# Performance work log

Hardware: AMD Instinct MI355X
Metric: run time of the kernel (lower is better)

Reference implementation:

```python
import jax, jax.numpy as jnp
from jax import lax
import numpy as np

LEVEL_HW = [(100, 100), (50, 50), (25, 25), (13, 13), (7, 7)]  # P3..P7 for 800x800 input
N, C, A, K, NCONV = 2, 256, 9, 80, 4
PRIOR_PROB = 0.01


def conv3x3(x, w, b):
    # x: (N,C,H,W), w: (O,I,3,3), stride 1, pad 1
    y = lax.conv_general_dilated(x, w, (1, 1), 'SAME',
                                 dimension_numbers=('NCHW', 'OIHW', 'NCHW'))
    return y + b[None, :, None, None]


def permute_to_N_HWA_K(t, k):
    # (N, A*k, H, W) -> (N, H*W*A, k), matching the torch helper
    n, _, h, w = t.shape
    return t.reshape(n, -1, k, h, w).transpose(0, 3, 4, 1, 2).reshape(n, -1, k)


def setup_inputs() -> dict:
    key = jax.random.key(0)
    ks = iter(jax.random.split(key, 64))
    inp = {}
    for i, (h, w) in enumerate(LEVEL_HW):
        inp[f"f{i}"] = jax.random.normal(next(ks), (N, C, h, w), jnp.float32)
    for pre in ("cls", "box"):
        for i in range(NCONV):
            inp[f"{pre}_w{i}"] = 0.01 * jax.random.normal(next(ks), (C, C, 3, 3), jnp.float32)
            inp[f"{pre}_b{i}"] = jnp.zeros((C,), jnp.float32)
    bias_value = -float(np.log((1.0 - PRIOR_PROB) / PRIOR_PROB))
    inp["cls_score_w"] = 0.01 * jax.random.normal(next(ks), (A * K, C, 3, 3), jnp.float32)
    inp["cls_score_b"] = jnp.full((A * K,), bias_value, jnp.float32)
    inp["box_pred_w"] = 0.01 * jax.random.normal(next(ks), (A * 4, C, 3, 3), jnp.float32)
    inp["box_pred_b"] = jnp.zeros((A * 4,), jnp.float32)
    return inp


def reference(f0, f1, f2, f3, f4,
              cls_w0, cls_b0, cls_w1, cls_b1, cls_w2, cls_b2, cls_w3, cls_b3,
              box_w0, box_b0, box_w1, box_b1, box_w2, box_b2, box_w3, box_b3,
              cls_score_w, cls_score_b, box_pred_w, box_pred_b):
    feats = [f0, f1, f2, f3, f4]
    cls_p = [(cls_w0, cls_b0), (cls_w1, cls_b1), (cls_w2, cls_b2), (cls_w3, cls_b3)]
    box_p = [(box_w0, box_b0), (box_w1, box_b1), (box_w2, box_b2), (box_w3, box_b3)]
    logits, boxes = [], []
    for f in feats:
        x = f
        for w, b in cls_p:
            x = jax.nn.relu(conv3x3(x, w, b))
        logits.append(permute_to_N_HWA_K(conv3x3(x, cls_score_w, cls_score_b), K))
        y = f
        for w, b in box_p:
            y = jax.nn.relu(conv3x3(y, w, b))
        boxes.append(permute_to_N_HWA_K(conv3x3(y, box_pred_w, box_pred_b), 4))
    # (N, R, K) and (N, R, 4) with R = sum_l Hl*Wl*A = 120087; concat on last dim
    return jnp.concatenate([jnp.concatenate(logits, 1), jnp.concatenate(boxes, 1)], axis=2)
```

## Files before the change

### kernel.cpp

```cpp
#include <hip/hip_runtime.h>


typedef __attribute__((ext_vector_type(8))) short short8;
typedef __attribute__((ext_vector_type(4))) float floatx4;

#define LVLTOT 14143

__device__ __forceinline__ unsigned short f2bf(float f) {
  unsigned int u = __float_as_uint(f);
  unsigned int r = (u + 0x7fffu + ((u >> 16) & 1u)) >> 16;
  return (unsigned short)r;
}

__device__ __forceinline__ void gload_lds16(const void* g, void* l) {
  __builtin_amdgcn_global_load_lds(
      (const __attribute__((address_space(1))) unsigned int*)g,
      (__attribute__((address_space(3))) unsigned int*)l, 16, 0, 0);
}

struct PrepArgs {
  const float* f[5];
  const float* w[10];
  unsigned short* wdst[10];
  int wblk_off[11];
  int cout[10];
  unsigned short* x0;
  unsigned short* bufA;
  unsigned short* bufB;
};

__global__ __launch_bounds__(256) void prep(PrepArgs A) {
  static const int Ht[5] = {100, 50, 25, 13, 7};
  static const int Wpt[5] = {102, 52, 27, 15, 9};
  static const int LOFFt[5] = {0, 10404, 13108, 13837, 14062};
  __shared__ float ts[32][33];
  const int bid = blockIdx.x;
  const int t = threadIdx.x;

  if (bid < 1090) {
    int sid = bid % 545, n = bid / 545;
    int l, h, wb;
    if (sid < 400)      { l = 0; h = sid >> 2; wb = sid & 3; }
    else if (sid < 500) { l = 1; h = (sid - 400) >> 1; wb = (sid - 400) & 1; }
    else if (sid < 525) { l = 2; h = sid - 500; wb = 0; }
    else if (sid < 538) { l = 3; h = sid - 525; wb = 0; }
    else                { l = 4; h = sid - 538; wb = 0; }
    const float* f = A.f[l];
    int H = Ht[l], W = H, Wp = Wpt[l], loff = LOFFt[l];
    int w0 = wb * 32;
    for (int s = 0; s < 8; s++) {
      int ch0 = s * 32;
      __syncthreads();
#pragma unroll
      for (int r4 = 0; r4 < 4; r4++) {
        int ch = ch0 + (t >> 5) + r4 * 8;
        int px = w0 + (t & 31);
        float v = 0.f;
        if (px < W) v = f[(((size_t)n * 256 + ch) * H + h) * W + px];
        ts[(t >> 5) + r4 * 8][t & 31] = v;
      }
      __syncthreads();
      int pxl = t >> 3, c4 = t & 7;
      if (w0 + pxl < W) {
        unsigned short pk[4];
#pragma unroll
        for (int k = 0; k < 4; k++) pk[k] = f2bf(ts[c4 * 4 + k][pxl]);
        *(unsigned long long*)(A.x0 +
            ((size_t)n * LVLTOT + loff + (size_t)(h + 1) * Wp + (w0 + pxl + 1)) *
                256 + ch0 + c4 * 4) = *(unsigned long long*)pk;
      }
    }
    return;
  }

  if (bid < 3970) {
    int b2 = bid - 1090;
    int tix = 0;
    while (b2 >= A.wblk_off[tix + 1]) tix++;
    int co = b2 - A.wblk_off[tix];
    int ci = t;
    bool valid = co < A.cout[tix];
    const float* w = A.w[tix];
    unsigned short* dst = A.wdst[tix];
    int cb = co >> 6, col = co & 63, chk = ci >> 5, qd = (ci >> 3) & 3, j = ci & 7;
#pragma unroll
    for (int tap = 0; tap < 9; tap++) {
      float v = valid ? w[((size_t)co * 256 + ci) * 9 + tap] : 0.f;
      dst[((((size_t)(cb * 8 + chk) * 9 + tap) * 4 + qd) * 64 + col) * 8 + j] =
          f2bf(v);
    }
    return;
  }

  {
    static const int BCUM[6] = {0, 404, 608, 712, 768, 800};
    int b3 = bid - 3970;
    int plane = b3 / 100;
    int item = (b3 % 100) * 256 + t;
    int pxi = item >> 5, oct = item & 31;
    if (pxi >= 800) return;
    int l = 0;
    while (pxi >= BCUM[l + 1]) l++;
    int j = pxi - BCUM[l];
    int Wp = Wpt[l];
    int r, c;
    if (j < Wp)            { r = 0; c = j; }
    else if (j < 2 * Wp)   { r = Wp - 1; c = j - Wp; }
    else { int k = j - 2 * Wp; r = 1 + (k >> 1); c = (k & 1) ? Wp - 1 : 0; }
    size_t px = (size_t)LOFFt[l] + (size_t)r * Wp + c;
    unsigned short* base = (plane < 4)
                               ? (A.bufA + (size_t)plane * LVLTOT * 256)
                               : (A.bufB + (size_t)(plane - 4) * LVLTOT * 256);
    floatx4 z;
    z[0] = z[1] = z[2] = z[3] = 0.f;
    *(floatx4*)(base + px * 256 + oct * 8) = z;
  }
}

__device__ __forceinline__ void decode_tile(int tile, int& l, int& h0, int& w0,
                                            int& H, int& W, int& Wp, int& loff) {
  const int Ht[5] = {100, 50, 25, 13, 7};
  const int Wpt[5] = {102, 52, 27, 15, 9};
  const int TXt[5] = {7, 4, 2, 1, 1};
  const int LOFFt[5] = {0, 10404, 13108, 13837, 14062};
  int tloc;
  if (tile < 49) { l = 0; tloc = tile; }
  else if (tile < 65) { l = 1; tloc = tile - 49; }
  else if (tile < 69) { l = 2; tloc = tile - 65; }
  else if (tile < 70) { l = 3; tloc = tile - 69; }
  else { l = 4; tloc = 0; }
  H = Ht[l]; W = H; Wp = Wpt[l]; loff = LOFFt[l];
  int ty = tloc / TXt[l], tx = tloc - ty * TXt[l];
  h0 = ty * 16; w0 = tx * 16;
}

#define CONV_MAIN_LOOP(INP, WBLOB, CB)                                         \
  {                                                                            \
    size_t xoff[6];                                                            \
    _Pragma("unroll") for (int g = 0; g < 6; g++) {                            \
      int px = g * 64 + lane;                                                  \
      int r = px / 18, c = px - r * 18;                                        \
      int hh = h0 + r; if (hh > Hpad - 1) hh = Hpad - 1;                       \
      int ww = w0 + c; if (ww > Wp - 1) ww = Wp - 1;                           \
      xoff[g] = ((size_t)hh * Wp + ww) * 256 + wv * 8;                         \
    }                                                                          \
    for (int ch = 0; ch < 8; ch++) {                                           \
      if (ch) __syncthreads();                                                 \
      const unsigned short* wsrc = (WBLOB) + ((size_t)((CB)*8 + ch)) * 18432;  \
      _Pragma("unroll") for (int i = 0; i < 9; i++)                            \
        gload_lds16(wsrc + i * 2048 + wv * 512 + lane * 8,                     \
                    lds_w + i * 2048 + wv * 512);                              \
      _Pragma("unroll") for (int g = 0; g < 6; g++)                            \
        gload_lds16((INP) + xoff[g] + ch * 32, lds_x + wv * 3072 + g * 512);   \
      __syncthreads();                                                         \
      const short8* xw = (const short8*)lds_w;                                 \
      const short8* xx = (const short8*)lds_x;                                 \
      _Pragma("unroll") for (int tdx = 0; tdx < 3; tdx++) {                    \
        short8 bfr[6];                                                         \
        _Pragma("unroll") for (int rw = 0; rw < 6; rw++)                       \
          bfr[rw] = xx[q * 384 + (wv * 4 + rw) * 18 + n16 + tdx];              \
        _Pragma("unroll") for (int tdy = 0; tdy < 3; tdy++) {                  \
          const int tap = tdy * 3 + tdx;                                       \
          _Pragma("unroll") for (int cc = 0; cc < 4; cc++) {                   \
            short8 afr = xw[(tap * 4 + q) * 64 + cc * 16 + n16];               \
            _Pragma("unroll") for (int rr = 0; rr < 4; rr++)                   \
              acc[cc][rr] = __builtin_amdgcn_mfma_f32_16x16x32_bf16(           \
                  afr, bfr[rr + tdy], acc[cc][rr], 0, 0, 0);                   \
          }                                                                    \
        }                                                                      \
      }                                                                        \
    }                                                                          \
  }

__global__ __launch_bounds__(256, 2) void conv_tower_mfma(
    const unsigned short* __restrict__ xin, unsigned short* __restrict__ xout,
    const unsigned short* __restrict__ wblob_cls,
    const unsigned short* __restrict__ wblob_box,
    const float* __restrict__ bias_cls, const float* __restrict__ bias_box,
    int in_n_stride, int in_tw_stride) {
  __shared__ __align__(16) unsigned short lds_w[18432];
  __shared__ __align__(16) unsigned short lds_x[12288];
  const int t = threadIdx.x, lane = t & 63, wv = t >> 6;
  const int q = lane >> 4, n16 = lane & 15;
  int l, h0, w0, H, W, Wp, loff;
  decode_tile(blockIdx.x, l, h0, w0, H, W, Wp, loff);
  const int Hpad = H + 2;
  const int cb = blockIdx.y;
  const int n = blockIdx.z >> 1, tw = blockIdx.z & 1;
  const unsigned short* wblob = tw ? wblob_box : wblob_cls;
  const float* bias = tw ? bias_box : bias_cls;
  const unsigned short* inp =
      xin + ((size_t)n * in_n_stride + (size_t)tw * in_tw_stride + loff) * 256;
  unsigned short* outp = xout + ((size_t)(n * 2 + tw) * LVLTOT + loff) * 256;

  floatx4 acc[4][4];
#pragma unroll
  for (int i = 0; i < 4; i++)
#pragma unroll
    for (int jj = 0; jj < 4; jj++) acc[i][jj] = (floatx4){0.f, 0.f, 0.f, 0.f};

  CONV_MAIN_LOOP(inp, wblob, cb)

#pragma unroll
  for (int cc = 0; cc < 4; cc++) {
    floatx4 bb = *(const floatx4*)(bias + cb * 64 + cc * 16 + q * 4);
#pragma unroll
    for (int rr = 0; rr < 4; rr++) {
      int h = h0 + wv * 4 + rr;
      int w_ = w0 + n16;
      if (h < H && w_ < W) {
        unsigned short pk[4];
#pragma unroll
        for (int rg = 0; rg < 4; rg++)
          pk[rg] = f2bf(fmaxf(acc[cc][rr][rg] + bb[rg], 0.f));
        size_t base =
            ((size_t)(h + 1) * Wp + (w_ + 1)) * 256 + cb * 64 + cc * 16 + q * 4;
        *(unsigned long long*)(outp + base) = *(unsigned long long*)pk;
      }
    }
  }
}

__global__ __launch_bounds__(256, 2) void conv_final_mfma(
    const unsigned short* __restrict__ xin, float* __restrict__ out,
    const unsigned short* __restrict__ wblob_cls,
    const unsigned short* __restrict__ wblob_box,
    const float* __restrict__ bias_cls, const float* __restrict__ bias_box) {
  __shared__ __align__(16) unsigned short lds_w[18432];
  __shared__ __align__(16) unsigned short lds_x[12288];
  const int t = threadIdx.x, lane = t & 63, wv = t >> 6;
  const int q = lane >> 4, n16 = lane & 15;
  int l, h0, w0, H, W, Wp, loff;
  decode_tile(blockIdx.x, l, h0, w0, H, W, Wp, loff);
  const int Hpad = H + 2;
  const int yb = blockIdx.y;
  const bool is_cls = yb < 12;
  const int cb = is_cls ? yb : 0;
  const int tw = is_cls ? 0 : 1;
  const int Cout = is_cls ? 720 : 36;
  const unsigned short* wblob = is_cls ? wblob_cls : wblob_box;
  const float* bias = is_cls ? bias_cls : bias_box;
  const int n = blockIdx.z;
  const int RB[5] = {0, 90000, 112500, 118125, 119646};
  const unsigned short* inp = xin + ((size_t)(n * 2 + tw) * LVLTOT + loff) * 256;

  floatx4 acc[4][4];
#pragma unroll
  for (int i = 0; i < 4; i++)
#pragma unroll
    for (int jj = 0; jj < 4; jj++) acc[i][jj] = (floatx4){0.f, 0.f, 0.f, 0.f};

  CONV_MAIN_LOOP(inp, wblob, cb)

#pragma unroll
  for (int cc = 0; cc < 4; cc++) {
    int co0 = cb * 64 + cc * 16 + q * 4;
    if (co0 >= Cout) continue;
    floatx4 bb = *(const floatx4*)(bias + co0);
    int a = is_cls ? (co0 / 80) : (co0 >> 2);
    int col0 = is_cls ? (co0 - a * 80) : 80;
#pragma unroll
    for (int rr = 0; rr < 4; rr++) {
      int h = h0 + wv * 4 + rr;
      int w_ = w0 + n16;
      if (h < H && w_ < W) {
        size_t ridx = (size_t)RB[l] + ((size_t)h * W + w_) * 9 + a;
        floatx4 v;
#pragma unroll
        for (int rg = 0; rg < 4; rg++) v[rg] = acc[cc][rr][rg] + bb[rg];
        *(floatx4*)(out + ((size_t)n * 120087 + ridx) * 84 + col0) = v;
      }
    }
  }
}

extern "C" void kernel_launch(void* const* d_in, const int* in_sizes, int n_in,
                              void* d_out, int out_size, void* d_ws,
                              size_t ws_size, hipStream_t stream) {
  char* ws = (char*)d_ws;
  unsigned short* bufB = (unsigned short*)(ws);
  unsigned short* X0 = (unsigned short*)(ws + 14482432);
  unsigned short* bufA = (unsigned short*)(ws + 28964864);
  unsigned short* tb[8];
  for (int i = 0; i < 8; i++)
    tb[i] = (unsigned short*)(ws + 57929728 + (size_t)i * 1179648);
  unsigned short* fb_cls = (unsigned short*)(ws + 67366912);
  unsigned short* fb_box = (unsigned short*)(ws + 70905856);

  float* out = (float*)d_out;

  PrepArgs pa;
  for (int i = 0; i < 5; i++) pa.f[i] = (const float*)d_in[i];
  for (int i = 0; i < 4; i++) {
    pa.w[i] = (const float*)d_in[5 + 2 * i];
    pa.w[4 + i] = (const float*)d_in[13 + 2 * i];
    pa.wdst[i] = tb[i];
    pa.wdst[4 + i] = tb[4 + i];
    pa.cout[i] = pa.cout[4 + i] = 256;
  }
  pa.w[8] = (const float*)d_in[21]; pa.wdst[8] = fb_cls; pa.cout[8] = 720;
  pa.w[9] = (const float*)d_in[23]; pa.wdst[9] = fb_box; pa.cout[9] = 36;
  int off = 0;
  for (int i = 0; i < 8; i++) { pa.wblk_off[i] = off; off += 256; }
  pa.wblk_off[8] = off; off += 768;
  pa.wblk_off[9] = off; off += 64;
  pa.wblk_off[10] = off;
  pa.x0 = X0;
  pa.bufA = bufA;
  pa.bufB = bufB;

  prep<<<dim3(4770), 256, 0, stream>>>(pa);

  const float *cls_b[4], *box_b[4];
  for (int i = 0; i < 4; i++) {
    cls_b[i] = (const float*)d_in[6 + 2 * i];
    box_b[i] = (const float*)d_in[14 + 2 * i];
  }

  dim3 gt(71, 4, 4);
  conv_tower_mfma<<<gt, 256, 0, stream>>>(X0, bufA, tb[0], tb[4], cls_b[0],
                                          box_b[0], LVLTOT, 0);
  conv_tower_mfma<<<gt, 256, 0, stream>>>(bufA, bufB, tb[1], tb[5], cls_b[1],
                                          box_b[1], 2 * LVLTOT, LVLTOT);
  conv_tower_mfma<<<gt, 256, 0, stream>>>(bufB, bufA, tb[2], tb[6], cls_b[2],
                                          box_b[2], 2 * LVLTOT, LVLTOT);
  conv_tower_mfma<<<gt, 256, 0, stream>>>(bufA, bufB, tb[3], tb[7], cls_b[3],
                                          box_b[3], 2 * LVLTOT, LVLTOT);

  conv_final_mfma<<<dim3(71, 13, 2), 256, 0, stream>>>(
      bufB, out, fb_cls, fb_box, (const float*)d_in[22], (const float*)d_in[24]);
}
```

Baseline: 638.5 us.

## Double-buffer LDS staging in conv main loop to overlap loads with MFMA

Splits the conv main loop into separate stage and compute macros and ping-pongs two LDS buffers, so the global-to-LDS loads for the next channel chunk are issued while MFMAs run on the current chunk. This halves the barriers per chunk pair and aims to hide global load latency. LDS use per block doubles to about 120 KB and the launch bounds drop the two-blocks-per-CU hint, so occupancy likely falls to one block per CU.

```diff
diff --git a/kernel.cpp b/kernel.cpp
--- a/kernel.cpp
+++ b/kernel.cpp
@@ -134,6 +134,37 @@
   h0 = ty * 16; w0 = tx * 16;
 }
 
+#define CONV_STAGE(INP, WBLOB, CB, CH, LW, LX)                                 \
+  {                                                                            \
+    const unsigned short* wsrc =                                               \
+        (WBLOB) + ((size_t)((CB) * 8 + (CH))) * 18432;                         \
+    _Pragma("unroll") for (int i = 0; i < 9; i++)                              \
+      gload_lds16(wsrc + i * 2048 + wv * 512 + lane * 8,                       \
+                  (LW) + i * 2048 + wv * 512);                                 \
+    _Pragma("unroll") for (int g = 0; g < 6; g++)                              \
+      gload_lds16((INP) + xoff[g] + (CH) * 32, (LX) + wv * 3072 + g * 512);    \
+  }
+
+#define CONV_COMPUTE(LW, LX)                                                   \
+  {                                                                            \
+    const short8* xw = (const short8*)(LW);                                    \
+    const short8* xx = (const short8*)(LX);                                    \
+    _Pragma("unroll") for (int tdx = 0; tdx < 3; tdx++) {                      \
+      short8 bfr[6];                                                           \
+      _Pragma("unroll") for (int rw = 0; rw < 6; rw++)                         \
+        bfr[rw] = xx[q * 384 + (wv * 4 + rw) * 18 + n16 + tdx];                \
+      _Pragma("unroll") for (int tdy = 0; tdy < 3; tdy++) {                    \
+        const int tap = tdy * 3 + tdx;                                         \
+        _Pragma("unroll") for (int cc = 0; cc < 4; cc++) {                     \
+          short8 afr = xw[(tap * 4 + q) * 64 + cc * 16 + n16];                 \
+          _Pragma("unroll") for (int rr = 0; rr < 4; rr++)                     \
+            acc[cc][rr] = __builtin_amdgcn_mfma_f32_16x16x32_bf16(             \
+                afr, bfr[rr + tdy], acc[cc][rr], 0, 0, 0);                     \
+        }                                                                      \
+      }                                                                        \
+    }                                                                          \
+  }
+
 #define CONV_MAIN_LOOP(INP, WBLOB, CB)                                         \
   {                                                                            \
     size_t xoff[6];                                                            \
@@ -144,42 +175,28 @@
       int ww = w0 + c; if (ww > Wp - 1) ww = Wp - 1;                           \
       xoff[g] = ((size_t)hh * Wp + ww) * 256 + wv * 8;                         \
     }                                                                          \
-    for (int ch = 0; ch < 8; ch++) {                                           \
-      if (ch) __syncthreads();                                                 \
-      const unsigned short* wsrc = (WBLOB) + ((size_t)((CB)*8 + ch)) * 18432;  \
-      _Pragma("unroll") for (int i = 0; i < 9; i++)                            \
-        gload_lds16(wsrc + i * 2048 + wv * 512 + lane * 8,                     \
-                    lds_w + i * 2048 + wv * 512);                              \
-      _Pragma("unroll") for (int g = 0; g < 6; g++)                            \
-        gload_lds16((INP) + xoff[g] + ch * 32, lds_x + wv * 3072 + g * 512);   \
+    CONV_STAGE(INP, WBLOB, CB, 0, lds_w[0], lds_x[0])                          \
+    __syncthreads();                                                           \
+    for (int cp = 0; cp < 4; cp++) {                                           \
+      CONV_STAGE(INP, WBLOB, CB, 2 * cp + 1, lds_w[1], lds_x[1])               \
+      CONV_COMPUTE(lds_w[0], lds_x[0])                                         \
       __syncthreads();                                                         \
-      const short8* xw = (const short8*)lds_w;                                 \
-      const short8* xx = (const short8*)lds_x;                                 \
-      _Pragma("unroll") for (int tdx = 0; tdx < 3; tdx++) {                    \
-        short8 bfr[6];                                                         \
-        _Pragma("unroll") for (int rw = 0; rw < 6; rw++)                       \
-          bfr[rw] = xx[q * 384 + (wv * 4 + rw) * 18 + n16 + tdx];              \
-        _Pragma("unroll") for (int tdy = 0; tdy < 3; tdy++) {                  \
-          const int tap = tdy * 3 + tdx;                                       \
-          _Pragma("unroll") for (int cc = 0; cc < 4; cc++) {                   \
-            short8 afr = xw[(tap * 4 + q) * 64 + cc * 16 + n16];               \
-            _Pragma("unroll") for (int rr = 0; rr < 4; rr++)                   \
-              acc[cc][rr] = __builtin_amdgcn_mfma_f32_16x16x32_bf16(           \
-                  afr, bfr[rr + tdy], acc[cc][rr], 0, 0, 0);                   \
-          }                                                                    \
-        }                                                                      \
+      if (cp < 3) {                                                            \
+        CONV_STAGE(INP, WBLOB, CB, 2 * cp + 2, lds_w[0], lds_x[0])             \
       }                                                                        \
+      CONV_COMPUTE(lds_w[1], lds_x[1])                                         \
+      __syncthreads();                                                         \
     }                                                                          \
   }
 
-__global__ __launch_bounds__(256, 2) void conv_tower_mfma(
+__global__ __launch_bounds__(256) void conv_tower_mfma(
     const unsigned short* __restrict__ xin, unsigned short* __restrict__ xout,
     const unsigned short* __restrict__ wblob_cls,
     const unsigned short* __restrict__ wblob_box,
     const float* __restrict__ bias_cls, const float* __restrict__ bias_box,
     int in_n_stride, int in_tw_stride) {
-  __shared__ __align__(16) unsigned short lds_w[18432];
-  __shared__ __align__(16) unsigned short lds_x[12288];
+  __shared__ __align__(16) unsigned short lds_w[2][18432];
+  __shared__ __align__(16) unsigned short lds_x[2][12288];
   const int t = threadIdx.x, lane = t & 63, wv = t >> 6;
   const int q = lane >> 4, n16 = lane & 15;
   int l, h0, w0, H, W, Wp, loff;
@@ -221,13 +238,13 @@
   }
 }
 
-__global__ __launch_bounds__(256, 2) void conv_final_mfma(
+__global__ __launch_bounds__(256) void conv_final_mfma(
     const unsigned short* __restrict__ xin, float* __restrict__ out,
     const unsigned short* __restrict__ wblob_cls,
     const unsigned short* __restrict__ wblob_box,
     const float* __restrict__ bias_cls, const float* __restrict__ bias_box) {
-  __shared__ __align__(16) unsigned short lds_w[18432];
-  __shared__ __align__(16) unsigned short lds_x[12288];
+  __shared__ __align__(16) unsigned short lds_w[2][18432];
+  __shared__ __align__(16) unsigned short lds_x[2][12288];
   const int t = threadIdx.x, lane = t & 63, wv = t >> 6;
   const int q = lane >> 4, n16 = lane & 15;
   int l, h0, w0, H, W, Wp, loff;
```

Result: slower. 854.3 us (+33.8%).

## Double-buffer LDS conv main loop with 512-thread 16x32 tiles

Applied to the files above, without the earlier changes.

The tile grows from 16x16 to 16x32 pixels, handled by 8 waves per block instead of 4, so each weight chunk staged in LDS is reused across twice as many pixels. The main loop now double-buffers weights and input in LDS and issues the next chunk's global-to-LDS loads interleaved with the three MFMA phases, using raw barriers, explicit waitcnts and setprio. The aim is to hide load latency and halve the weight traffic per output. The cost is about 154KB of LDS per block, which limits occupancy to one block per CU, and fewer blocks overall, which may leave CUs idle on small levels.

```diff
diff --git a/kernel.cpp b/kernel.cpp
--- a/kernel.cpp
+++ b/kernel.cpp
@@ -121,67 +121,129 @@
                                             int& H, int& W, int& Wp, int& loff) {
   const int Ht[5] = {100, 50, 25, 13, 7};
   const int Wpt[5] = {102, 52, 27, 15, 9};
-  const int TXt[5] = {7, 4, 2, 1, 1};
+  const int TXt[5] = {4, 2, 1, 1, 1};
   const int LOFFt[5] = {0, 10404, 13108, 13837, 14062};
   int tloc;
-  if (tile < 49) { l = 0; tloc = tile; }
-  else if (tile < 65) { l = 1; tloc = tile - 49; }
-  else if (tile < 69) { l = 2; tloc = tile - 65; }
-  else if (tile < 70) { l = 3; tloc = tile - 69; }
+  if (tile < 28) { l = 0; tloc = tile; }
+  else if (tile < 36) { l = 1; tloc = tile - 28; }
+  else if (tile < 38) { l = 2; tloc = tile - 36; }
+  else if (tile < 39) { l = 3; tloc = tile - 38; }
   else { l = 4; tloc = 0; }
   H = Ht[l]; W = H; Wp = Wpt[l]; loff = LOFFt[l];
   int ty = tloc / TXt[l], tx = tloc - ty * TXt[l];
-  h0 = ty * 16; w0 = tx * 16;
-}
+  h0 = ty * 16; w0 = tx * 32;
+}
+
+#define BARX() __builtin_amdgcn_s_barrier()
+#define SFEN() __builtin_amdgcn_sched_barrier(0)
+#define LGKM0() asm volatile("s_waitcnt lgkmcnt(0)" ::: "memory")
+#define VMC0() asm volatile("s_waitcnt vmcnt(0)" ::: "memory")
+
+#define CONV_PHASE(P, STAGE)                                                   \
+  {                                                                            \
+    short8 bfr[6];                                                             \
+    _Pragma("unroll") for (int rb = 0; rb < 6; rb++)                           \
+      bfr[rb] = lx8[q * 640 + (R4 + rb) * 34 + cwn + (P)];                     \
+    short8 afr[3][4];                                                          \
+    _Pragma("unroll") for (int ty_ = 0; ty_ < 3; ty_++)                        \
+      _Pragma("unroll") for (int cA = 0; cA < 4; cA++)                         \
+        afr[ty_][cA] = lw8[((ty_ * 3 + (P)) * 4 + q) * 64 + cA * 16 + n16];    \
+    STAGE                                                                      \
+    SFEN();                                                                    \
+    BARX();                                                                    \
+    LGKM0();                                                                   \
+    SFEN();                                                                    \
+    __builtin_amdgcn_s_setprio(1);                                             \
+    _Pragma("unroll") for (int ty_ = 0; ty_ < 3; ty_++)                        \
+      _Pragma("unroll") for (int cA = 0; cA < 4; cA++)                         \
+        _Pragma("unroll") for (int rr = 0; rr < 4; rr++)                       \
+          acc[cA][rr] = __builtin_amdgcn_mfma_f32_16x16x32_bf16(               \
+              afr[ty_][cA], bfr[rr + ty_], acc[cA][rr], 0, 0, 0);              \
+    __builtin_amdgcn_s_setprio(0);                                             \
+    SFEN();                                                                    \
+  }
+
+#define SG_X(K, CH32, DST)                                                     \
+  gload_lds16((INP_) + xsrc[K] + (CH32),                                       \
+              (DST) + ((size_t)qx * 640 + (sgb + (K)) * 64) * 8)
+#define SG_W(K, SRC, DST)                                                      \
+  {                                                                            \
+    int g_ = wv + 8 * (K);                                                     \
+    if (g_ < 36)                                                               \
+      gload_lds16((SRC) + (size_t)g_ * 512 + lane * 8,                         \
+                  (DST) + (size_t)g_ * 512);                                   \
+  }
 
 #define CONV_MAIN_LOOP(INP, WBLOB, CB)                                         \
   {                                                                            \
-    size_t xoff[6];                                                            \
-    _Pragma("unroll") for (int g = 0; g < 6; g++) {                            \
-      int px = g * 64 + lane;                                                  \
-      int r = px / 18, c = px - r * 18;                                        \
-      int hh = h0 + r; if (hh > Hpad - 1) hh = Hpad - 1;                       \
-      int ww = w0 + c; if (ww > Wp - 1) ww = Wp - 1;                           \
-      xoff[g] = ((size_t)hh * Wp + ww) * 256 + wv * 8;                         \
+    const unsigned short* INP_ = (INP);                                        \
+    const int qx = wv & 3, sgb = (wv >> 2) * 5;                                \
+    int xsrc[5];                                                               \
+    _Pragma("unroll") for (int k = 0; k < 5; k++) {                            \
+      int p = (sgb + k) * 64 + lane;                                           \
+      if (p > 611) p = 611;                                                    \
+      int r_ = p / 34, c_ = p - r_ * 34;                                       \
+      int hh = h0 + r_; if (hh > Hpad - 1) hh = Hpad - 1;                      \
+      int ww = w0 + c_; if (ww > Wp - 1) ww = Wp - 1;                          \
+      xsrc[k] = (hh * Wp + ww) * 256 + qx * 8;                                 \
     }                                                                          \
-    for (int ch = 0; ch < 8; ch++) {                                           \
-      if (ch) __syncthreads();                                                 \
-      const unsigned short* wsrc = (WBLOB) + ((size_t)((CB)*8 + ch)) * 18432;  \
-      _Pragma("unroll") for (int i = 0; i < 9; i++)                            \
-        gload_lds16(wsrc + i * 2048 + wv * 512 + lane * 8,                     \
-                    lds_w + i * 2048 + wv * 512);                              \
-      _Pragma("unroll") for (int g = 0; g < 6; g++)                            \
-        gload_lds16((INP) + xoff[g] + ch * 32, lds_x + wv * 3072 + g * 512);   \
-      __syncthreads();                                                         \
-      const short8* xw = (const short8*)lds_w;                                 \
-      const short8* xx = (const short8*)lds_x;                                 \
-      _Pragma("unroll") for (int tdx = 0; tdx < 3; tdx++) {                    \
-        short8 bfr[6];                                                         \
-        _Pragma("unroll") for (int rw = 0; rw < 6; rw++)                       \
-          bfr[rw] = xx[q * 384 + (wv * 4 + rw) * 18 + n16 + tdx];              \
-        _Pragma("unroll") for (int tdy = 0; tdy < 3; tdy++) {                  \
-          const int tap = tdy * 3 + tdx;                                       \
-          _Pragma("unroll") for (int cc = 0; cc < 4; cc++) {                   \
-            short8 afr = xw[(tap * 4 + q) * 64 + cc * 16 + n16];               \
-            _Pragma("unroll") for (int rr = 0; rr < 4; rr++)                   \
-              acc[cc][rr] = __builtin_amdgcn_mfma_f32_16x16x32_bf16(           \
-                  afr, bfr[rr + tdy], acc[cc][rr], 0, 0, 0);                   \
-          }                                                                    \
+    unsigned short* lwc = &lds_w[0][0];                                        \
+    unsigned short* lwn = &lds_w[1][0];                                        \
+    unsigned short* lxc = &lds_x[0][0];                                        \
+    unsigned short* lxn = &lds_x[1][0];                                        \
+    {                                                                          \
+      const unsigned short* wsrc0 = (WBLOB) + (size_t)((CB) * 8) * 18432;      \
+      _Pragma("unroll") for (int k = 0; k < 5; k++) SG_X(k, 0, lxc);           \
+      _Pragma("unroll") for (int k = 0; k < 5; k++) SG_W(k, wsrc0, lwc);       \
+    }                                                                          \
+    VMC0();                                                                    \
+    BARX();                                                                    \
+    _Pragma("unroll 1") for (int c = 0; c < 8; c++) {                          \
+      const unsigned short* wsrc =                                             \
+          (WBLOB) + (size_t)((CB) * 8 + c + 1) * 18432;                        \
+      const int ch32 = (c + 1) * 32;                                           \
+      const bool st = (c < 7);                                                 \
+      const short8* lw8 = (const short8*)lwc;                                  \
+      const short8* lx8 = (const short8*)lxc;                                  \
+      CONV_PHASE(0, {                                                          \
+        if (st) {                                                              \
+          SG_X(0, ch32, lxn); SG_X(1, ch32, lxn);                              \
+          SG_W(0, wsrc, lwn); SG_W(1, wsrc, lwn);                              \
         }                                                                      \
-      }                                                                        \
+      })                                                                       \
+      BARX();                                                                  \
+      CONV_PHASE(1, {                                                          \
+        if (st) {                                                              \
+          SG_X(2, ch32, lxn); SG_X(3, ch32, lxn);                              \
+          SG_W(2, wsrc, lwn); SG_W(3, wsrc, lwn);                              \
+        }                                                                      \
+      })                                                                       \
+      BARX();                                                                  \
+      CONV_PHASE(2, {                                                          \
+        if (st) {                                                              \
+          SG_X(4, ch32, lxn);                                                  \
+          SG_W(4, wsrc, lwn);                                                  \
+        }                                                                      \
+      })                                                                       \
+      VMC0();                                                                  \
+      BARX();                                                                  \
+      unsigned short* tp_;                                                     \
+      tp_ = lwc; lwc = lwn; lwn = tp_;                                         \
+      tp_ = lxc; lxc = lxn; lxn = tp_;                                         \
     }                                                                          \
   }
 
-__global__ __launch_bounds__(256, 2) void conv_tower_mfma(
+__global__ __launch_bounds__(512, 2) void conv_tower_mfma(
     const unsigned short* __restrict__ xin, unsigned short* __restrict__ xout,
     const unsigned short* __restrict__ wblob_cls,
     const unsigned short* __restrict__ wblob_box,
     const float* __restrict__ bias_cls, const float* __restrict__ bias_box,
     int in_n_stride, int in_tw_stride) {
-  __shared__ __align__(16) unsigned short lds_w[18432];
-  __shared__ __align__(16) unsigned short lds_x[12288];
+  __shared__ __align__(16) unsigned short lds_w[2][18432];
+  __shared__ __align__(16) unsigned short lds_x[2][20480];
   const int t = threadIdx.x, lane = t & 63, wv = t >> 6;
   const int q = lane >> 4, n16 = lane & 15;
+  const int R4 = (wv >> 1) * 4, cwn = (wv & 1) * 16 + n16;
   int l, h0, w0, H, W, Wp, loff;
   decode_tile(blockIdx.x, l, h0, w0, H, W, Wp, loff);
   const int Hpad = H + 2;
@@ -202,34 +264,35 @@
   CONV_MAIN_LOOP(inp, wblob, cb)
 
 #pragma unroll
-  for (int cc = 0; cc < 4; cc++) {
-    floatx4 bb = *(const floatx4*)(bias + cb * 64 + cc * 16 + q * 4);
+  for (int cA = 0; cA < 4; cA++) {
+    floatx4 bb = *(const floatx4*)(bias + cb * 64 + cA * 16 + q * 4);
 #pragma unroll
     for (int rr = 0; rr < 4; rr++) {
-      int h = h0 + wv * 4 + rr;
-      int w_ = w0 + n16;
+      int h = h0 + R4 + rr;
+      int w_ = w0 + cwn;
       if (h < H && w_ < W) {
         unsigned short pk[4];
 #pragma unroll
         for (int rg = 0; rg < 4; rg++)
-          pk[rg] = f2bf(fmaxf(acc[cc][rr][rg] + bb[rg], 0.f));
+          pk[rg] = f2bf(fmaxf(acc[cA][rr][rg] + bb[rg], 0.f));
         size_t base =
-            ((size_t)(h + 1) * Wp + (w_ + 1)) * 256 + cb * 64 + cc * 16 + q * 4;
+            ((size_t)(h + 1) * Wp + (w_ + 1)) * 256 + cb * 64 + cA * 16 + q * 4;
         *(unsigned long long*)(outp + base) = *(unsigned long long*)pk;
       }
     }
   }
 }
 
-__global__ __launch_bounds__(256, 2) void conv_final_mfma(
+__global__ __launch_bounds__(512, 2) void conv_final_mfma(
     const unsigned short* __restrict__ xin, float* __restrict__ out,
     const unsigned short* __restrict__ wblob_cls,
     const unsigned short* __restrict__ wblob_box,
     const float* __restrict__ bias_cls, const float* __restrict__ bias_box) {
-  __shared__ __align__(16) unsigned short lds_w[18432];
-  __shared__ __align__(16) unsigned short lds_x[12288];
+  __shared__ __align__(16) unsigned short lds_w[2][18432];
+  __shared__ __align__(16) unsigned short lds_x[2][20480];
   const int t = threadIdx.x, lane = t & 63, wv = t >> 6;
   const int q = lane >> 4, n16 = lane & 15;
+  const int R4 = (wv >> 1) * 4, cwn = (wv & 1) * 16 + n16;
   int l, h0, w0, H, W, Wp, loff;
   decode_tile(blockIdx.x, l, h0, w0, H, W, Wp, loff);
   const int Hpad = H + 2;
@@ -253,21 +316,21 @@
   CONV_MAIN_LOOP(inp, wblob, cb)
 
 #pragma unroll
-  for (int cc = 0; cc < 4; cc++) {
-    int co0 = cb * 64 + cc * 16 + q * 4;
+  for (int cA = 0; cA < 4; cA++) {
+    int co0 = cb * 64 + cA * 16 + q * 4;
     if (co0 >= Cout) continue;
     floatx4 bb = *(const floatx4*)(bias + co0);
     int a = is_cls ? (co0 / 80) : (co0 >> 2);
     int col0 = is_cls ? (co0 - a * 80) : 80;
 #pragma unroll
     for (int rr = 0; rr < 4; rr++) {
-      int h = h0 + wv * 4 + rr;
-      int w_ = w0 + n16;
+      int h = h0 + R4 + rr;
+      int w_ = w0 + cwn;
       if (h < H && w_ < W) {
         size_t ridx = (size_t)RB[l] + ((size_t)h * W + w_) * 9 + a;
         floatx4 v;
 #pragma unroll
-        for (int rg = 0; rg < 4; rg++) v[rg] = acc[cc][rr][rg] + bb[rg];
+        for (int rg = 0; rg < 4; rg++) v[rg] = acc[cA][rr][rg] + bb[rg];
         *(floatx4*)(out + ((size_t)n * 120087 + ridx) * 84 + col0) = v;
       }
     }
@@ -317,16 +380,16 @@
     box_b[i] = (const float*)d_in[14 + 2 * i];
   }
 
-  dim3 gt(71, 4, 4);
-  conv_tower_mfma<<<gt, 256, 0, stream>>>(X0, bufA, tb[0], tb[4], cls_b[0],
+  dim3 gt(40, 4, 4);
+  conv_tower_mfma<<<gt, 512, 0, stream>>>(X0, bufA, tb[0], tb[4], cls_b[0],
                                           box_b[0], LVLTOT, 0);
-  conv_tower_mfma<<<gt, 256, 0, stream>>>(bufA, bufB, tb[1], tb[5], cls_b[1],
+  conv_tower_mfma<<<gt, 512, 0, stream>>>(bufA, bufB, tb[1], tb[5], cls_b[1],
                                           box_b[1], 2 * LVLTOT, LVLTOT);
-  conv_tower_mfma<<<gt, 256, 0, stream>>>(bufB, bufA, tb[2], tb[6], cls_b[2],
+  conv_tower_mfma<<<gt, 512, 0, stream>>>(bufB, bufA, tb[2], tb[6], cls_b[2],
                                           box_b[2], 2 * LVLTOT, LVLTOT);
-  conv_tower_mfma<<<gt, 256, 0, stream>>>(bufA, bufB, tb[3], tb[7], cls_b[3],
+  conv_tower_mfma<<<gt, 512, 0, stream>>>(bufA, bufB, tb[3], tb[7], cls_b[3],
                                           box_b[3], 2 * LVLTOT, LVLTOT);
 
-  conv_final_mfma<<<dim3(71, 13, 2), 256, 0, stream>>>(
+  conv_final_mfma<<<dim3(40, 13, 2), 512, 0, stream>>>(
       bufB, out, fb_cls, fb_box, (const float*)d_in[22], (const float*)d_in[24]);
 }
```

Measured after the change: 705.9 us. 10.5% more time.

## Enlarge conv spatial tile to 32x16 rows for more weight reuse

Applied to the files above, without the earlier changes.

Doubles the spatial tile height from 16 to 32 rows, so each wave computes 8 output rows instead of 4 and reuses every weight fragment across twice as many MFMAs. The input halo staging is rewritten to load 34x18 pixels for all four channel quarters, using a flat per-thread index. The tile grid shrinks from 71 to 40 tiles per level set. The cost is more accumulator registers (128 floats), a larger LDS footprint per block, fewer blocks and possibly lower occupancy, and more wasted work at the edges of the small levels.

```diff
diff --git a/kernel.cpp b/kernel.cpp
--- a/kernel.cpp
+++ b/kernel.cpp
@@ -124,48 +124,51 @@
   const int TXt[5] = {7, 4, 2, 1, 1};
   const int LOFFt[5] = {0, 10404, 13108, 13837, 14062};
   int tloc;
-  if (tile < 49) { l = 0; tloc = tile; }
-  else if (tile < 65) { l = 1; tloc = tile - 49; }
-  else if (tile < 69) { l = 2; tloc = tile - 65; }
-  else if (tile < 70) { l = 3; tloc = tile - 69; }
+  if (tile < 28) { l = 0; tloc = tile; }
+  else if (tile < 36) { l = 1; tloc = tile - 28; }
+  else if (tile < 38) { l = 2; tloc = tile - 36; }
+  else if (tile < 39) { l = 3; tloc = tile - 38; }
   else { l = 4; tloc = 0; }
   H = Ht[l]; W = H; Wp = Wpt[l]; loff = LOFFt[l];
   int ty = tloc / TXt[l], tx = tloc - ty * TXt[l];
-  h0 = ty * 16; w0 = tx * 16;
+  h0 = ty * 32; w0 = tx * 16;
 }
 
 #define CONV_MAIN_LOOP(INP, WBLOB, CB)                                         \
   {                                                                            \
-    size_t xoff[6];                                                            \
-    _Pragma("unroll") for (int g = 0; g < 6; g++) {                            \
-      int px = g * 64 + lane;                                                  \
-      int r = px / 18, c = px - r * 18;                                        \
-      int hh = h0 + r; if (hh > Hpad - 1) hh = Hpad - 1;                       \
-      int ww = w0 + c; if (ww > Wp - 1) ww = Wp - 1;                           \
-      xoff[g] = ((size_t)hh * Wp + ww) * 256 + wv * 8;                         \
+    int xsrc[10];                                                              \
+    _Pragma("unroll") for (int k = 0; k < 10; k++) {                           \
+      int u = k * 256 + t;                                                     \
+      if (u > 2447) u = 2447;                                                  \
+      int qq = u / 612, sl = u - qq * 612;                                     \
+      int r_ = sl / 18, c_ = sl - r_ * 18;                                     \
+      int hh = h0 + r_; if (hh > Hpad - 1) hh = Hpad - 1;                      \
+      int ww = w0 + c_; if (ww > Wp - 1) ww = Wp - 1;                          \
+      xsrc[k] = (hh * Wp + ww) * 256 + qq * 8;                                 \
     }                                                                          \
-    for (int ch = 0; ch < 8; ch++) {                                           \
+    _Pragma("unroll 1") for (int ch = 0; ch < 8; ch++) {                       \
       if (ch) __syncthreads();                                                 \
       const unsigned short* wsrc = (WBLOB) + ((size_t)((CB)*8 + ch)) * 18432;  \
       _Pragma("unroll") for (int i = 0; i < 9; i++)                            \
         gload_lds16(wsrc + i * 2048 + wv * 512 + lane * 8,                     \
                     lds_w + i * 2048 + wv * 512);                              \
-      _Pragma("unroll") for (int g = 0; g < 6; g++)                            \
-        gload_lds16((INP) + xoff[g] + ch * 32, lds_x + wv * 3072 + g * 512);   \
+      _Pragma("unroll") for (int k = 0; k < 10; k++)                           \
+        gload_lds16((INP) + xsrc[k] + ch * 32,                                 \
+                    lds_x + (size_t)(k * 256 + wv * 64) * 8);                  \
       __syncthreads();                                                         \
       const short8* xw = (const short8*)lds_w;                                 \
       const short8* xx = (const short8*)lds_x;                                 \
       _Pragma("unroll") for (int tdx = 0; tdx < 3; tdx++) {                    \
-        short8 bfr[6];                                                         \
-        _Pragma("unroll") for (int rw = 0; rw < 6; rw++)                       \
-          bfr[rw] = xx[q * 384 + (wv * 4 + rw) * 18 + n16 + tdx];              \
+        short8 bfr[10];                                                        \
+        _Pragma("unroll") for (int rb = 0; rb < 10; rb++)                      \
+          bfr[rb] = xx[q * 612 + (wv * 8 + rb) * 18 + n16 + tdx];              \
         _Pragma("unroll") for (int tdy = 0; tdy < 3; tdy++) {                  \
           const int tap = tdy * 3 + tdx;                                       \
-          _Pragma("unroll") for (int cc = 0; cc < 4; cc++) {                   \
-            short8 afr = xw[(tap * 4 + q) * 64 + cc * 16 + n16];               \
-            _Pragma("unroll") for (int rr = 0; rr < 4; rr++)                   \
-              acc[cc][rr] = __builtin_amdgcn_mfma_f32_16x16x32_bf16(           \
-                  afr, bfr[rr + tdy], acc[cc][rr], 0, 0, 0);                   \
+          _Pragma("unroll") for (int cA = 0; cA < 4; cA++) {                   \
+            short8 afr = xw[(tap * 4 + q) * 64 + cA * 16 + n16];               \
+            _Pragma("unroll") for (int rr = 0; rr < 8; rr++)                   \
+              acc[cA][rr] = __builtin_amdgcn_mfma_f32_16x16x32_bf16(           \
+                  afr, bfr[rr + tdy], acc[cA][rr], 0, 0, 0);                   \
           }                                                                    \
         }                                                                      \
       }                                                                        \
@@ -179,7 +182,7 @@
     const float* __restrict__ bias_cls, const float* __restrict__ bias_box,
     int in_n_stride, int in_tw_stride) {
   __shared__ __align__(16) unsigned short lds_w[18432];
-  __shared__ __align__(16) unsigned short lds_x[12288];
+  __shared__ __align__(16) unsigned short lds_x[20480];
   const int t = threadIdx.x, lane = t & 63, wv = t >> 6;
   const int q = lane >> 4, n16 = lane & 15;
   int l, h0, w0, H, W, Wp, loff;
@@ -193,28 +196,28 @@
       xin + ((size_t)n * in_n_stride + (size_t)tw * in_tw_stride + loff) * 256;
   unsigned short* outp = xout + ((size_t)(n * 2 + tw) * LVLTOT + loff) * 256;
 
-  floatx4 acc[4][4];
+  floatx4 acc[4][8];
 #pragma unroll
   for (int i = 0; i < 4; i++)
 #pragma unroll
-    for (int jj = 0; jj < 4; jj++) acc[i][jj] = (floatx4){0.f, 0.f, 0.f, 0.f};
+    for (int jj = 0; jj < 8; jj++) acc[i][jj] = (floatx4){0.f, 0.f, 0.f, 0.f};
 
   CONV_MAIN_LOOP(inp, wblob, cb)
 
 #pragma unroll
-  for (int cc = 0; cc < 4; cc++) {
-    floatx4 bb = *(const floatx4*)(bias + cb * 64 + cc * 16 + q * 4);
-#pragma unroll
-    for (int rr = 0; rr < 4; rr++) {
-      int h = h0 + wv * 4 + rr;
+  for (int cA = 0; cA < 4; cA++) {
+    floatx4 bb = *(const floatx4*)(bias + cb * 64 + cA * 16 + q * 4);
+#pragma unroll
+    for (int rr = 0; rr < 8; rr++) {
+      int h = h0 + wv * 8 + rr;
       int w_ = w0 + n16;
       if (h < H && w_ < W) {
         unsigned short pk[4];
 #pragma unroll
         for (int rg = 0; rg < 4; rg++)
-          pk[rg] = f2bf(fmaxf(acc[cc][rr][rg] + bb[rg], 0.f));
+          pk[rg] = f2bf(fmaxf(acc[cA][rr][rg] + bb[rg], 0.f));
         size_t base =
-            ((size_t)(h + 1) * Wp + (w_ + 1)) * 256 + cb * 64 + cc * 16 + q * 4;
+            ((size_t)(h + 1) * Wp + (w_ + 1)) * 256 + cb * 64 + cA * 16 + q * 4;
         *(unsigned long long*)(outp + base) = *(unsigned long long*)pk;
       }
     }
@@ -227,7 +230,7 @@
     const unsigned short* __restrict__ wblob_box,
     const float* __restrict__ bias_cls, const float* __restrict__ bias_box) {
   __shared__ __align__(16) unsigned short lds_w[18432];
-  __shared__ __align__(16) unsigned short lds_x[12288];
+  __shared__ __align__(16) unsigned short lds_x[20480];
   const int t = threadIdx.x, lane = t & 63, wv = t >> 6;
   const int q = lane >> 4, n16 = lane & 15;
   int l, h0, w0, H, W, Wp, loff;
@@ -244,30 +247,30 @@
   const int RB[5] = {0, 90000, 112500, 118125, 119646};
   const unsigned short* inp = xin + ((size_t)(n * 2 + tw) * LVLTOT + loff) * 256;
 
-  floatx4 acc[4][4];
+  floatx4 acc[4][8];
 #pragma unroll
   for (int i = 0; i < 4; i++)
 #pragma unroll
-    for (int jj = 0; jj < 4; jj++) acc[i][jj] = (floatx4){0.f, 0.f, 0.f, 0.f};
+    for (int jj = 0; jj < 8; jj++) acc[i][jj] = (floatx4){0.f, 0.f, 0.f, 0.f};
 
   CONV_MAIN_LOOP(inp, wblob, cb)
 
 #pragma unroll
-  for (int cc = 0; cc < 4; cc++) {
-    int co0 = cb * 64 + cc * 16 + q * 4;
+  for (int cA = 0; cA < 4; cA++) {
+    int co0 = cb * 64 + cA * 16 + q * 4;
     if (co0 >= Cout) continue;
     floatx4 bb = *(const floatx4*)(bias + co0);
     int a = is_cls ? (co0 / 80) : (co0 >> 2);
     int col0 = is_cls ? (co0 - a * 80) : 80;
 #pragma unroll
-    for (int rr = 0; rr < 4; rr++) {
-      int h = h0 + wv * 4 + rr;
+    for (int rr = 0; rr < 8; rr++) {
+      int h = h0 + wv * 8 + rr;
       int w_ = w0 + n16;
       if (h < H && w_ < W) {
         size_t ridx = (size_t)RB[l] + ((size_t)h * W + w_) * 9 + a;
         floatx4 v;
 #pragma unroll
-        for (int rg = 0; rg < 4; rg++) v[rg] = acc[cc][rr][rg] + bb[rg];
+        for (int rg = 0; rg < 4; rg++) v[rg] = acc[cA][rr][rg] + bb[rg];
         *(floatx4*)(out + ((size_t)n * 120087 + ridx) * 84 + col0) = v;
       }
     }
@@ -317,7 +320,7 @@
     box_b[i] = (const float*)d_in[14 + 2 * i];
   }
 
-  dim3 gt(71, 4, 4);
+  dim3 gt(40, 4, 4);
   conv_tower_mfma<<<gt, 256, 0, stream>>>(X0, bufA, tb[0], tb[4], cls_b[0],
                                           box_b[0], LVLTOT, 0);
   conv_tower_mfma<<<gt, 256, 0, stream>>>(bufA, bufB, tb[1], tb[5], cls_b[1],
@@ -327,6 +330,6 @@
   conv_tower_mfma<<<gt, 256, 0, stream>>>(bufA, bufB, tb[3], tb[7], cls_b[3],
                                           box_b[3], 2 * LVLTOT, LVLTOT);
 
-  conv_final_mfma<<<dim3(71, 13, 2), 256, 0, stream>>>(
+  conv_final_mfma<<<dim3(40, 13, 2), 256, 0, stream>>>(
       bufB, out, fb_cls, fb_box, (const float*)d_in[22], (const float*)d_in[24]);
 }
```

Result: slower. 768.0 us (+20.3%).
